# Kernel optimization log

Hardware: AMD Instinct MI355X
Metric: run time of the kernel (lower is better)

## Reference

```python
import jax, jax.numpy as jnp
import numpy as np

H = 64  # hidden size (matched to ~22K params per the module docstring)


def _lstm_cell(h, c, x, W_ih, W_hh, b):
    # PyTorch gate order: i, f, g, o. x: [B, in], h/c: [B, H]
    gates = x @ W_ih.T + h @ W_hh.T + b            # [B, 4H]
    i, f, g, o = jnp.split(gates, 4, axis=-1)
    i = jax.nn.sigmoid(i)
    f = jax.nn.sigmoid(f)
    g = jnp.tanh(g)
    o = jax.nn.sigmoid(o)
    c_new = f * c + i * g
    h_new = o * jnp.tanh(c_new)
    return h_new, c_new


def setup_inputs() -> dict:
    key = jax.random.key(0)
    ks = jax.random.split(key, 12)
    B, T = 2048, 512
    k = 1.0 / np.sqrt(H)  # PyTorch LSTM/Linear init bound
    u = lambda kk, shape: jax.random.uniform(kk, shape, jnp.float32, -k, k)
    return {
        "context": jax.random.normal(ks[0], (B, T), jnp.float32),
        "W_ih_enc": u(ks[1], (4 * H, 1)),
        "W_hh_enc": u(ks[2], (4 * H, H)),
        "b_ih_enc": u(ks[3], (4 * H,)),
        "b_hh_enc": u(ks[4], (4 * H,)),
        "W_ih_dec": u(ks[5], (4 * H, 1)),
        "W_hh_dec": u(ks[6], (4 * H, H)),
        "b_ih_dec": u(ks[7], (4 * H,)),
        "b_hh_dec": u(ks[8], (4 * H,)),
        "W_head": u(ks[9], (1, H)),
        "b_head": u(ks[10], (1,)),
        "n_steps": 256,
    }


def reference(context, W_ih_enc, W_hh_enc, b_ih_enc, b_hh_enc,
              W_ih_dec, W_hh_dec, b_ih_dec, b_hh_dec,
              W_head, b_head, n_steps):
    B = context.shape[0]
    dt = context.dtype
    b_enc = b_ih_enc + b_hh_enc
    b_dec = b_ih_dec + b_hh_dec

    # --- encode context step-by-step (batch_first LSTM over T) ---
    def enc_step(carry, x_t):  # x_t: [B]
        h, c = carry
        h, c = _lstm_cell(h, c, x_t[:, None], W_ih_enc, W_hh_enc, b_enc)
        return (h, c), None

    h0 = jnp.zeros((B, H), dt)
    c0 = jnp.zeros((B, H), dt)
    (h, c), _ = jax.lax.scan(enc_step, (h0, c0), context.T)  # scan over T

    z0 = context[:, -1:]  # [B, 1] last context value

    def dec_step(carry, _):
        h_d, c_d, z = carry
        h_d, c_d = _lstm_cell(h_d, c_d, z, W_ih_dec, W_hh_dec, b_dec)
        z_next = h_d @ W_head.T + b_head  # [B, 1]
        return (h_d, c_d, z_next), z_next[:, 0]

    _, preds = jax.lax.scan(dec_step, (h, c, z0), None, length=n_steps)  # [n_steps, B]
    return preds.T  # [B, n_steps]
```

## Files before the change

kernel.cpp:

```cpp
#include <hip/hip_runtime.h>
#include <cstddef>
#include <cstdint>

#define TMAX 512
#define HDIM 64

typedef _Float16 half2v __attribute__((ext_vector_type(2)));

__device__ __forceinline__ float fsig(float x) {
    x = fminf(fmaxf(x, -30.f), 30.f);
    float e = __expf(-x);
    return __builtin_amdgcn_rcpf(1.f + e);
}
__device__ __forceinline__ float ftanh(float x) {
    x = fminf(fmaxf(x, -15.f), 15.f);
    float e = __expf(2.f * x);
    return (e - 1.f) * __builtin_amdgcn_rcpf(e + 1.f);
}

#if __has_builtin(__builtin_amdgcn_fdot2)
__device__ __forceinline__ float dot2acc(half2v a, half2v b, float c) {
    return __builtin_amdgcn_fdot2(a, b, c, false);
}
#else
__device__ __forceinline__ float dot2acc(half2v a, half2v b, float c) {
    return fmaf((float)a.y, (float)b.y, fmaf((float)a.x, (float)b.x, c));
}
#endif

__global__ __launch_bounds__(64, 2)
void lstm_wave_kernel(const float* __restrict__ ctx_g,
                      const float* __restrict__ Wih_e,
                      const float* __restrict__ Whh_e,
                      const float* __restrict__ bih_e,
                      const float* __restrict__ bhh_e,
                      const float* __restrict__ Wih_d,
                      const float* __restrict__ Whh_d,
                      const float* __restrict__ bih_d,
                      const float* __restrict__ bhh_d,
                      const float* __restrict__ Whead,
                      const float* __restrict__ bhead,
                      float* __restrict__ out,
                      int T, int n_steps)
{
    __shared__ __align__(16) float    ctx_s[TMAX];
    __shared__ __align__(16) _Float16 h_s[HDIM];

    const int lane = threadIdx.x;
    const int row  = blockIdx.x;

    const float* ctxr = ctx_g + (size_t)row * T;
    for (int t = lane; t < T; t += 64) ctx_s[t] = ctxr[t];

    uint32_t wbits[4][32];
    float    wih[4], bias[4];

    #pragma unroll
    for (int g = 0; g < 4; ++g) {
        const int j = lane + (g << 6);
        const float2* wr = reinterpret_cast<const float2*>(Whh_e + (size_t)j * HDIM);
        #pragma unroll
        for (int k = 0; k < 32; ++k) {
            float2 wv = wr[k];
            half2v hw = half2v{(_Float16)wv.x, (_Float16)wv.y};
            wbits[g][k] = __builtin_bit_cast(uint32_t, hw);
        }
        wih[g]  = Wih_e[j];
        bias[g] = bih_e[j] + bhh_e[j];
    }
    #pragma unroll
    for (int g = 0; g < 4; ++g) {
        #pragma unroll
        for (int k = 0; k < 32; ++k) asm volatile("" : "+v"(wbits[g][k]));
        asm volatile("" : "+v"(wih[g]), "+v"(bias[g]));
    }

    float c = 0.f, h = 0.f;
    h_s[lane] = (_Float16)0.f;

    for (int t = 0; t < T; ++t) {
        const float x = ctx_s[t];
        float aA[4], aB[4];
        #pragma unroll
        for (int g = 0; g < 4; ++g) { aA[g] = fmaf(x, wih[g], bias[g]); aB[g] = 0.f; }
        #pragma unroll
        for (int ch = 0; ch < 8; ++ch) {
            uint4 hv = reinterpret_cast<const uint4*>(h_s)[ch];
            half2v hp[4];
            hp[0] = __builtin_bit_cast(half2v, hv.x);
            hp[1] = __builtin_bit_cast(half2v, hv.y);
            hp[2] = __builtin_bit_cast(half2v, hv.z);
            hp[3] = __builtin_bit_cast(half2v, hv.w);
            #pragma unroll
            for (int e = 0; e < 4; ++e) {
                const int k = ch * 4 + e;
                #pragma unroll
                for (int g = 0; g < 4; ++g) {
                    half2v wv = __builtin_bit_cast(half2v, wbits[g][k]);
                    if (ch < 4) aA[g] = dot2acc(wv, hp[e], aA[g]);
                    else        aB[g] = dot2acc(wv, hp[e], aB[g]);
                }
            }
        }
        const float ig = fsig(aA[0] + aB[0]);
        const float fg = fsig(aA[1] + aB[1]);
        const float gg = ftanh(aA[2] + aB[2]);
        const float og = fsig(aA[3] + aB[3]);
        c = fmaf(fg, c, ig * gg);
        h = og * ftanh(c);
        h_s[lane] = (_Float16)h;
    }

    #pragma unroll
    for (int g = 0; g < 4; ++g) {
        const int j = lane + (g << 6);
        const float2* wr = reinterpret_cast<const float2*>(Whh_d + (size_t)j * HDIM);
        #pragma unroll
        for (int k = 0; k < 32; ++k) {
            float2 wv = wr[k];
            half2v hw = half2v{(_Float16)wv.x, (_Float16)wv.y};
            wbits[g][k] = __builtin_bit_cast(uint32_t, hw);
        }
        wih[g]  = Wih_d[j];
        bias[g] = bih_d[j] + bhh_d[j];
    }
    #pragma unroll
    for (int g = 0; g < 4; ++g) {
        #pragma unroll
        for (int k = 0; k < 32; ++k) asm volatile("" : "+v"(wbits[g][k]));
        asm volatile("" : "+v"(wih[g]), "+v"(bias[g]));
    }
    const float wh = Whead[lane];
    const float bh = bhead[0];
    float z = ctx_s[T - 1];

    for (int s = 0; s < n_steps; ++s) {
        float aA[4], aB[4];
        #pragma unroll
        for (int g = 0; g < 4; ++g) { aA[g] = fmaf(z, wih[g], bias[g]); aB[g] = 0.f; }
        #pragma unroll
        for (int ch = 0; ch < 8; ++ch) {
            uint4 hv = reinterpret_cast<const uint4*>(h_s)[ch];
            half2v hp[4];
            hp[0] = __builtin_bit_cast(half2v, hv.x);
            hp[1] = __builtin_bit_cast(half2v, hv.y);
            hp[2] = __builtin_bit_cast(half2v, hv.z);
            hp[3] = __builtin_bit_cast(half2v, hv.w);
            #pragma unroll
            for (int e = 0; e < 4; ++e) {
                const int k = ch * 4 + e;
                #pragma unroll
                for (int g = 0; g < 4; ++g) {
                    half2v wv = __builtin_bit_cast(half2v, wbits[g][k]);
                    if (ch < 4) aA[g] = dot2acc(wv, hp[e], aA[g]);
                    else        aB[g] = dot2acc(wv, hp[e], aB[g]);
                }
            }
        }
        const float ig = fsig(aA[0] + aB[0]);
        const float fg = fsig(aA[1] + aB[1]);
        const float gg = ftanh(aA[2] + aB[2]);
        const float og = fsig(aA[3] + aB[3]);
        c = fmaf(fg, c, ig * gg);
        h = og * ftanh(c);
        h_s[lane] = (_Float16)h;

        float p = h * wh;
        #pragma unroll
        for (int off = 32; off >= 1; off >>= 1)
            p += __shfl_xor(p, off);
        z = p + bh;
        if (lane == 0) out[(size_t)row * n_steps + s] = z;
    }
}

extern "C" void kernel_launch(void* const* d_in, const int* in_sizes, int n_in,
                              void* d_out, int out_size, void* d_ws, size_t ws_size,
                              hipStream_t stream)
{
    const float* ctx   = (const float*)d_in[0];
    const float* Wih_e = (const float*)d_in[1];
    const float* Whh_e = (const float*)d_in[2];
    const float* bih_e = (const float*)d_in[3];
    const float* bhh_e = (const float*)d_in[4];
    const float* Wih_d = (const float*)d_in[5];
    const float* Whh_d = (const float*)d_in[6];
    const float* bih_d = (const float*)d_in[7];
    const float* bhh_d = (const float*)d_in[8];
    const float* Whead = (const float*)d_in[9];
    const float* bhead = (const float*)d_in[10];
    float* out = (float*)d_out;

    const int B = 2048;
    const int T = in_sizes[0] / B;
    const int n_steps = out_size / B;

    lstm_wave_kernel<<<dim3(B), dim3(64), 0, stream>>>(
        ctx, Wih_e, Whh_e, bih_e, bhh_e,
        Wih_d, Whh_d, bih_d, bhh_d,
        Whead, bhead, out, T, n_steps);
}
```

Measured before the change: 639.3 us.

## Split LSTM gate rows across two waves per batch row with LDS exchange

Each batch row now runs on two 64-lane waves instead of one. Wave 0 computes the i and f gates and wave 1 computes the g and o gates, each holding half the recurrent weights in registers. Wave 1 passes its activated gates through shared memory, and wave 0 updates c and h and computes the head output. This halves the dot-product work per wave on the serial recurrence and cuts register pressure, which allows higher occupancy. The cost is two block barriers per timestep plus the shared-memory exchange, and wave 1 sits idle during the cell update.

```diff
diff --git a/kernel.cpp b/kernel.cpp
--- a/kernel.cpp
+++ b/kernel.cpp
@@ -28,61 +28,62 @@
 }
 #endif
 
-__global__ __launch_bounds__(64, 2)
-void lstm_wave_kernel(const float* __restrict__ ctx_g,
-                      const float* __restrict__ Wih_e,
-                      const float* __restrict__ Whh_e,
-                      const float* __restrict__ bih_e,
-                      const float* __restrict__ bhh_e,
-                      const float* __restrict__ Wih_d,
-                      const float* __restrict__ Whh_d,
-                      const float* __restrict__ bih_d,
-                      const float* __restrict__ bhh_d,
-                      const float* __restrict__ Whead,
-                      const float* __restrict__ bhead,
-                      float* __restrict__ out,
-                      int T, int n_steps)
+__global__ __launch_bounds__(128, 4)
+void lstm_2wave_kernel(const float* __restrict__ ctx_g,
+                       const float* __restrict__ Wih_e,
+                       const float* __restrict__ Whh_e,
+                       const float* __restrict__ bih_e,
+                       const float* __restrict__ bhh_e,
+                       const float* __restrict__ Wih_d,
+                       const float* __restrict__ Whh_d,
+                       const float* __restrict__ bih_d,
+                       const float* __restrict__ bhh_d,
+                       const float* __restrict__ Whead,
+                       const float* __restrict__ bhead,
+                       float* __restrict__ out,
+                       int T, int n_steps)
 {
     __shared__ __align__(16) float    ctx_s[TMAX];
     __shared__ __align__(16) _Float16 h_s[HDIM];
-
-    const int lane = threadIdx.x;
+    __shared__ __align__(16) float2   exch[HDIM];
+    __shared__ float z_s;
+
+    const int tid  = threadIdx.x;
+    const int u    = tid & 63;
+    const int wid  = tid >> 6;
     const int row  = blockIdx.x;
 
     const float* ctxr = ctx_g + (size_t)row * T;
-    for (int t = lane; t < T; t += 64) ctx_s[t] = ctxr[t];
-
-    uint32_t wbits[4][32];
-    float    wih[4], bias[4];
-
-    #pragma unroll
-    for (int g = 0; g < 4; ++g) {
-        const int j = lane + (g << 6);
-        const float2* wr = reinterpret_cast<const float2*>(Whh_e + (size_t)j * HDIM);
+    for (int t = tid; t < T; t += 128) ctx_s[t] = ctxr[t];
+
+    const int j0 = u + (wid << 7);
+    const int j1 = j0 + 64;
+
+    uint32_t w0[32], w1[32];
+    float wih0, wih1, b0, b1;
+
+    {
+        const float2* r0 = reinterpret_cast<const float2*>(Whh_e + (size_t)j0 * HDIM);
+        const float2* r1 = reinterpret_cast<const float2*>(Whh_e + (size_t)j1 * HDIM);
         #pragma unroll
         for (int k = 0; k < 32; ++k) {
-            float2 wv = wr[k];
-            half2v hw = half2v{(_Float16)wv.x, (_Float16)wv.y};
-            wbits[g][k] = __builtin_bit_cast(uint32_t, hw);
-        }
-        wih[g]  = Wih_e[j];
-        bias[g] = bih_e[j] + bhh_e[j];
-    }
-    #pragma unroll
-    for (int g = 0; g < 4; ++g) {
-        #pragma unroll
-        for (int k = 0; k < 32; ++k) asm volatile("" : "+v"(wbits[g][k]));
-        asm volatile("" : "+v"(wih[g]), "+v"(bias[g]));
-    }
-
-    float c = 0.f, h = 0.f;
-    h_s[lane] = (_Float16)0.f;
+            float2 a = r0[k], b = r1[k];
+            w0[k] = __builtin_bit_cast(uint32_t, half2v{(_Float16)a.x, (_Float16)a.y});
+            w1[k] = __builtin_bit_cast(uint32_t, half2v{(_Float16)b.x, (_Float16)b.y});
+        }
+        wih0 = Wih_e[j0];  wih1 = Wih_e[j1];
+        b0 = bih_e[j0] + bhh_e[j0];
+        b1 = bih_e[j1] + bhh_e[j1];
+    }
+
+    float c = 0.f;
+    if (wid == 0) h_s[u] = (_Float16)0.f;
+    __syncthreads();
 
     for (int t = 0; t < T; ++t) {
         const float x = ctx_s[t];
-        float aA[4], aB[4];
-        #pragma unroll
-        for (int g = 0; g < 4; ++g) { aA[g] = fmaf(x, wih[g], bias[g]); aB[g] = 0.f; }
+        float a0A = fmaf(x, wih0, b0), a0B = 0.f;
+        float a1A = fmaf(x, wih1, b1), a1B = 0.f;
         #pragma unroll
         for (int ch = 0; ch < 8; ++ch) {
             uint4 hv = reinterpret_cast<const uint4*>(h_s)[ch];
@@ -94,50 +95,48 @@
             #pragma unroll
             for (int e = 0; e < 4; ++e) {
                 const int k = ch * 4 + e;
-                #pragma unroll
-                for (int g = 0; g < 4; ++g) {
-                    half2v wv = __builtin_bit_cast(half2v, wbits[g][k]);
-                    if (ch < 4) aA[g] = dot2acc(wv, hp[e], aA[g]);
-                    else        aB[g] = dot2acc(wv, hp[e], aB[g]);
-                }
+                half2v wv0 = __builtin_bit_cast(half2v, w0[k]);
+                half2v wv1 = __builtin_bit_cast(half2v, w1[k]);
+                if (ch < 4) { a0A = dot2acc(wv0, hp[e], a0A); a1A = dot2acc(wv1, hp[e], a1A); }
+                else        { a0B = dot2acc(wv0, hp[e], a0B); a1B = dot2acc(wv1, hp[e], a1B); }
             }
         }
-        const float ig = fsig(aA[0] + aB[0]);
-        const float fg = fsig(aA[1] + aB[1]);
-        const float gg = ftanh(aA[2] + aB[2]);
-        const float og = fsig(aA[3] + aB[3]);
-        c = fmaf(fg, c, ig * gg);
-        h = og * ftanh(c);
-        h_s[lane] = (_Float16)h;
-    }
-
-    #pragma unroll
-    for (int g = 0; g < 4; ++g) {
-        const int j = lane + (g << 6);
-        const float2* wr = reinterpret_cast<const float2*>(Whh_d + (size_t)j * HDIM);
+        const float a0 = a0A + a0B;
+        const float a1 = a1A + a1B;
+        if (wid) {
+            exch[u] = make_float2(ftanh(a0), fsig(a1));
+        }
+        __syncthreads();
+        if (!wid) {
+            const float ii = fsig(a0);
+            const float ff = fsig(a1);
+            const float2 go = exch[u];
+            c = fmaf(ff, c, ii * go.x);
+            h_s[u] = (_Float16)(go.y * ftanh(c));
+        }
+        __syncthreads();
+    }
+
+    {
+        const float2* r0 = reinterpret_cast<const float2*>(Whh_d + (size_t)j0 * HDIM);
+        const float2* r1 = reinterpret_cast<const float2*>(Whh_d + (size_t)j1 * HDIM);
         #pragma unroll
         for (int k = 0; k < 32; ++k) {
-            float2 wv = wr[k];
-            half2v hw = half2v{(_Float16)wv.x, (_Float16)wv.y};
-            wbits[g][k] = __builtin_bit_cast(uint32_t, hw);
-        }
-        wih[g]  = Wih_d[j];
-        bias[g] = bih_d[j] + bhh_d[j];
-    }
-    #pragma unroll
-    for (int g = 0; g < 4; ++g) {
-        #pragma unroll
-        for (int k = 0; k < 32; ++k) asm volatile("" : "+v"(wbits[g][k]));
-        asm volatile("" : "+v"(wih[g]), "+v"(bias[g]));
-    }
-    const float wh = Whead[lane];
+            float2 a = r0[k], b = r1[k];
+            w0[k] = __builtin_bit_cast(uint32_t, half2v{(_Float16)a.x, (_Float16)a.y});
+            w1[k] = __builtin_bit_cast(uint32_t, half2v{(_Float16)b.x, (_Float16)b.y});
+        }
+        wih0 = Wih_d[j0];  wih1 = Wih_d[j1];
+        b0 = bih_d[j0] + bhh_d[j0];
+        b1 = bih_d[j1] + bhh_d[j1];
+    }
+    const float wh = Whead[u];
     const float bh = bhead[0];
     float z = ctx_s[T - 1];
 
     for (int s = 0; s < n_steps; ++s) {
-        float aA[4], aB[4];
-        #pragma unroll
-        for (int g = 0; g < 4; ++g) { aA[g] = fmaf(z, wih[g], bias[g]); aB[g] = 0.f; }
+        float a0A = fmaf(z, wih0, b0), a0B = 0.f;
+        float a1A = fmaf(z, wih1, b1), a1B = 0.f;
         #pragma unroll
         for (int ch = 0; ch < 8; ++ch) {
             uint4 hv = reinterpret_cast<const uint4*>(h_s)[ch];
@@ -149,28 +148,37 @@
             #pragma unroll
             for (int e = 0; e < 4; ++e) {
                 const int k = ch * 4 + e;
-                #pragma unroll
-                for (int g = 0; g < 4; ++g) {
-                    half2v wv = __builtin_bit_cast(half2v, wbits[g][k]);
-                    if (ch < 4) aA[g] = dot2acc(wv, hp[e], aA[g]);
-                    else        aB[g] = dot2acc(wv, hp[e], aB[g]);
-                }
+                half2v wv0 = __builtin_bit_cast(half2v, w0[k]);
+                half2v wv1 = __builtin_bit_cast(half2v, w1[k]);
+                if (ch < 4) { a0A = dot2acc(wv0, hp[e], a0A); a1A = dot2acc(wv1, hp[e], a1A); }
+                else        { a0B = dot2acc(wv0, hp[e], a0B); a1B = dot2acc(wv1, hp[e], a1B); }
             }
         }
-        const float ig = fsig(aA[0] + aB[0]);
-        const float fg = fsig(aA[1] + aB[1]);
-        const float gg = ftanh(aA[2] + aB[2]);
-        const float og = fsig(aA[3] + aB[3]);
-        c = fmaf(fg, c, ig * gg);
-        h = og * ftanh(c);
-        h_s[lane] = (_Float16)h;
-
-        float p = h * wh;
-        #pragma unroll
-        for (int off = 32; off >= 1; off >>= 1)
-            p += __shfl_xor(p, off);
-        z = p + bh;
-        if (lane == 0) out[(size_t)row * n_steps + s] = z;
+        const float a0 = a0A + a0B;
+        const float a1 = a1A + a1B;
+        if (wid) {
+            exch[u] = make_float2(ftanh(a0), fsig(a1));
+        }
+        __syncthreads();
+        if (!wid) {
+            const float ii = fsig(a0);
+            const float ff = fsig(a1);
+            const float2 go = exch[u];
+            c = fmaf(ff, c, ii * go.x);
+            const float h = go.y * ftanh(c);
+            h_s[u] = (_Float16)h;
+            float p = h * wh;
+            #pragma unroll
+            for (int off = 32; off >= 1; off >>= 1)
+                p += __shfl_xor(p, off);
+            if (u == 0) {
+                const float zn = p + bh;
+                z_s = zn;
+                out[(size_t)row * n_steps + s] = zn;
+            }
+        }
+        __syncthreads();
+        z = z_s;
     }
 }
 
@@ -195,7 +203,7 @@
     const int T = in_sizes[0] / B;
     const int n_steps = out_size / B;
 
-    lstm_wave_kernel<<<dim3(B), dim3(64), 0, stream>>>(
+    lstm_2wave_kernel<<<dim3(B), dim3(128), 0, stream>>>(
         ctx, Wih_e, Whh_e, bih_e, bhh_e,
         Wih_d, Whh_d, bih_d, bhh_d,
         Whead, bhead, out, T, n_steps);
```

New measurement: 785.8 us. 22.9% more time.
